# Kernel tuning notes

Measured on AMD Instinct MI355X. Metric: run time of the kernel, lower is better.

The kernel has to match this reference:

```python
import jax, jax.numpy as jnp
import numpy as np

N_NODES = 100000
N_EDGES = 1600000
NUM_FEATURES = 128
HIDDEN = 64
NUM_CLASSES = 16


def setup_inputs() -> dict:
    key = jax.random.key(0)
    k1, k2, k3, k4 = jax.random.split(key, 4)
    x = jax.random.normal(k1, (N_NODES, NUM_FEATURES), dtype=jnp.float32)
    edge_index = jax.random.randint(k2, (2, N_EDGES), 0, N_NODES, dtype=jnp.int64)
    # Glorot-ish scaled weights ([in, out] layout; PyG stores [out,in] but math is x @ W)
    W1 = jax.random.normal(k3, (NUM_FEATURES, HIDDEN), dtype=jnp.float32) * (1.0 / np.sqrt(NUM_FEATURES))
    W2 = jax.random.normal(k4, (HIDDEN, NUM_CLASSES), dtype=jnp.float32) * (1.0 / np.sqrt(HIDDEN))
    return {"x": x, "edge_index": edge_index, "W1": W1, "W2": W2}


def _gcn_conv(x, edge_index, W):
    # GCNConv(add_self_loops=False, bias=False): linear then sym-normalized scatter-add.
    n = x.shape[0]
    row, col = edge_index[0], edge_index[1]  # source -> target
    h = x @ W  # [N, out]
    # degree from unit edge weights scattered on target nodes
    deg = jax.ops.segment_sum(jnp.ones(row.shape[0], dtype=h.dtype), col, num_segments=n)
    deg_inv_sqrt = jnp.where(deg > 0, jax.lax.rsqrt(jnp.maximum(deg, 1.0)), 0.0)
    norm = deg_inv_sqrt[row] * deg_inv_sqrt[col]  # [E]
    msg = h[row] * norm[:, None]  # gather + scale, [E, out]
    return jax.ops.segment_sum(msg, col, num_segments=n)  # scatter-add to targets


def reference(x, edge_index, W1, W2):
    h = _gcn_conv(x, edge_index, W1)
    h = _gcn_conv(h, edge_index, W2)
    return jax.nn.log_softmax(h, axis=1)
```

## Files before the change

### kernel.cpp

```cpp
#include <hip/hip_runtime.h>
#include <hip/hip_bf16.h>
#include <hip/hip_fp16.h>


#define STRIDE 48
#define BCAP   3072


__global__ __launch_bounds__(256) void k_bucket(const int* __restrict__ ei,
                                                const void* __restrict__ xv,
                                                const void* __restrict__ W1v,
                                                const void* __restrict__ W2v,
                                                int* __restrict__ flags,
                                                float* __restrict__ W12,
                                                int* __restrict__ bcnt,
                                                int* __restrict__ buf,
                                                int e, int n, int nb) {
    __shared__ int hist[1024];
    __shared__ int basec[1024];
    __shared__ float wtmp[2048];
    __shared__ int sraw, sbad;
    int t = threadIdx.x;
    int b = blockIdx.x;

    if (t == 0) { sraw = 0; sbad = 0; }
    for (int i = t; i < nb; i += 256) hist[i] = 0;
    __syncthreads();

    {
        int i = b * 2048 + t;
        if (i < e && ei[2 * (size_t)i + 1] != 0) atomicOr(&sraw, 1);
    }
    if (b < 8) {
        const unsigned short* xs = (const unsigned short*)xv;
        int bad = 0;
        for (int i = t; i < 1024; i += 256) {
            unsigned ex2 = (xs[i] >> 7) & 0xFF;
            if (ex2 >= 0x90) bad = 1;
        }
        if (bad) atomicOr(&sbad, 1);
    }
    __syncthreads();
    int raw = sraw ? 0 : 1;

    if (b < 8) {
        bool f32 = sbad != 0;
        if (f32) {
            const float* W1 = (const float*)W1v;
            const float* W2 = (const float*)W2v;
            for (int i = t; i < 1024; i += 256) {
                wtmp[i] = W1[b * 1024 + i];
                wtmp[1024 + i] = W2[i];
            }
        } else {
            const __hip_bfloat16* W1 = (const __hip_bfloat16*)W1v;
            const __hip_bfloat16* W2 = (const __hip_bfloat16*)W2v;
            for (int i = t; i < 1024; i += 256) {
                wtmp[i] = __bfloat162float(W1[b * 1024 + i]);
                wtmp[1024 + i] = __bfloat162float(W2[i]);
            }
        }
    }

    int e0 = b * 2048;
    int bk[8], rec[8];
#pragma unroll
    for (int j = 0; j < 8; ++j) {
        int i = e0 + j * 256 + t;
        bk[j] = -1;
        if (i < e) {
            int r, c;
            if (raw) {
                r = ((const int2*)ei)[(size_t)i].x;
                c = ((const int2*)ei)[(size_t)e + i].x;
            } else {
                r = ei[i];
                c = ei[(size_t)e + i];
            }
            if ((unsigned)c < (unsigned)n && (unsigned)r < (unsigned)n) {
                bk[j] = c >> 7;
                rec[j] = ((c & 127) << 17) | r;
                atomicAdd(&hist[bk[j]], 1);
            }
        }
    }
    __syncthreads();

    if (b < 8) {
        int kl = t >> 4, c = t & 15;
        float acc = 0.0f;
#pragma unroll 8
        for (int f = 0; f < 64; ++f) acc += wtmp[kl * 64 + f] * wtmp[1024 + f * 16 + c];
        W12[(16 * b + kl) * 16 + c] = acc;
        if (b == 0 && t == 0) { flags[0] = sbad; flags[1] = raw; }
    }

    for (int i = t; i < nb; i += 256) {
        int h = hist[i];
        basec[i] = h ? atomicAdd(&bcnt[i], h) : 0;
    }
    __syncthreads();
#pragma unroll
    for (int j = 0; j < 8; ++j) {
        if (bk[j] >= 0) {
            int slot = atomicAdd(&basec[bk[j]], 1);
            if (slot < BCAP) buf[(size_t)bk[j] * BCAP + slot] = rec[j];
        }
    }
}


__global__ __launch_bounds__(256) void k_csr_z(const int* __restrict__ bcnt,
                                               const int* __restrict__ buf,
                                               const void* __restrict__ xv,
                                               const float* __restrict__ W12,
                                               const int* __restrict__ flags,
                                               int* __restrict__ cnt,
                                               int* __restrict__ csr,
                                               __half* __restrict__ z, int n) {
    __shared__ int lcnt[128];
    __shared__ int lcsr[128 * STRIDE];
    __shared__ float ws[2048];
    int t = threadIdx.x;
    int b = blockIdx.x;
    if (t < 128) lcnt[t] = 0;
    int4 zero4 = {0, 0, 0, 0};
    for (int i = t; i < 128 * STRIDE / 4; i += 256) ((int4*)lcsr)[i] = zero4;
    for (int i = t; i < 2048; i += 256) ws[i] = W12[i];
    __syncthreads();

    int m = bcnt[b];
    if (m > BCAP) m = BCAP;
    for (int i = t; i < m; i += 256) {
        int rec = buf[(size_t)b * BCAP + i];
        int cl = rec >> 17;
        int r = rec & 0x1FFFF;
        int slot = atomicAdd(&lcnt[cl], 1);
        if (slot < STRIDE) lcsr[cl * STRIDE + slot] = r;
    }
    __syncthreads();

    {
        int node = (b << 7) + t;
        if (t < 128 && node < n) cnt[node] = lcnt[t];
    }
    const int4* src = (const int4*)lcsr;
    int4* dst = (int4*)csr + (size_t)b * (128 * STRIDE / 4);
    for (int i = t; i < 128 * STRIDE / 4; i += 256) dst[i] = src[i];

    int node_l = t >> 1;
    int kh = t & 1;
    int node0 = (b << 7) + node_l;
    if (node0 >= n) return;
    int node = node0;

    float acc[16];
#pragma unroll
    for (int c = 0; c < 16; ++c) acc[c] = 0.0f;

    if (flags[0]) {
        const float4* x4 = (const float4*)xv + (size_t)node * 32 + kh * 16;
#pragma unroll
        for (int j = 0; j < 16; ++j) {
            float4 v = x4[j];
            float xk[4] = {v.x, v.y, v.z, v.w};
#pragma unroll
            for (int q = 0; q < 4; ++q) {
                const float* w = &ws[(kh * 64 + j * 4 + q) * 16];
                float xx = xk[q];
#pragma unroll
                for (int c = 0; c < 16; ++c) acc[c] += xx * w[c];
            }
        }
    } else {
        const uint4* x4 = (const uint4*)xv + (size_t)node * 16 + kh * 8;
#pragma unroll
        for (int j = 0; j < 8; ++j) {
            uint4 v = x4[j];
            float xk[8];
            xk[0] = __uint_as_float(v.x << 16);
            xk[1] = __uint_as_float(v.x & 0xffff0000u);
            xk[2] = __uint_as_float(v.y << 16);
            xk[3] = __uint_as_float(v.y & 0xffff0000u);
            xk[4] = __uint_as_float(v.z << 16);
            xk[5] = __uint_as_float(v.z & 0xffff0000u);
            xk[6] = __uint_as_float(v.w << 16);
            xk[7] = __uint_as_float(v.w & 0xffff0000u);
#pragma unroll
            for (int q = 0; q < 8; ++q) {
                const float* w = &ws[(kh * 64 + j * 8 + q) * 16];
                float xx = xk[q];
#pragma unroll
                for (int c = 0; c < 16; ++c) acc[c] += xx * w[c];
            }
        }
    }

#pragma unroll
    for (int c = 0; c < 16; ++c) acc[c] += __shfl_xor(acc[c], 1);

    int deg = lcnt[node_l];
    float di = (deg > 0) ? rsqrtf((float)deg) : 0.0f;
    int c0 = kh * 8;
    __half2 hh[4];
#pragma unroll
    for (int j = 0; j < 4; ++j)
        hh[j] = __halves2half2(__float2half(acc[c0 + 2 * j] * di),
                               __float2half(acc[c0 + 2 * j + 1] * di));
    uint4 u;
    u.x = *(unsigned*)&hh[0]; u.y = *(unsigned*)&hh[1];
    u.z = *(unsigned*)&hh[2]; u.w = *(unsigned*)&hh[3];
    ((uint4*)(z + (size_t)node * 16))[kh] = u;
}


__global__ __launch_bounds__(256) void k_agg1b(const int* __restrict__ cnt,
                                               const int* __restrict__ csr,
                                               const __half* __restrict__ z,
                                               __half* __restrict__ z2, int n) {
    int t = threadIdx.x;
    int wid = t >> 6, lane = t & 63;
    int half = lane >> 5, l5 = lane & 31;
    int node0 = blockIdx.x * 8 + wid * 2 + half;
    int node = node0 < n ? node0 : n - 1;
    int id  = csr[(size_t)node * STRIDE + l5];
    int id2 = csr[(size_t)node * STRIDE + 32 + (l5 & 15)];
    int deg = cnt[node];
    float di = (deg > 0) ? rsqrtf((float)deg) : 0.0f;
    int m = deg < STRIDE ? deg : STRIDE;
    int sub = l5 >> 3, f2 = l5 & 7;
    int base = half << 5;
    const __half2* zp = (const __half2*)z;
    float ax = 0.0f, ay = 0.0f;
#pragma unroll
    for (int j = 0; j < 24; j += 4) {
        int s = __shfl(id, base + j + sub);
        float2 v = __half22float2(zp[(size_t)s * 8 + f2]);
        bool ok = (j + sub) < m;
        ax += ok ? v.x : 0.0f;
        ay += ok ? v.y : 0.0f;
    }
    for (int j = 24; j < m; j += 4) {
        int sidx = j + sub;
        int s = (j < 32) ? __shfl(id, base + sidx)
                         : __shfl(id2, base + (sidx & 15));
        if (sidx < m) {
            float2 v = __half22float2(zp[(size_t)s * 8 + f2]);
            ax += v.x;
            ay += v.y;
        }
    }
    ax += __shfl_xor(ax, 8);  ay += __shfl_xor(ay, 8);
    ax += __shfl_xor(ax, 16); ay += __shfl_xor(ay, 16);
    float s2 = di * di;
    if (node0 < n && l5 < 8)
        ((__half2*)z2)[(size_t)node * 8 + l5] =
            __halves2half2(__float2half(ax * s2), __float2half(ay * s2));
}


__global__ __launch_bounds__(256) void k_agg2b(const int* __restrict__ cnt,
                                               const int* __restrict__ csr,
                                               const __half* __restrict__ z2,
                                               const int* __restrict__ flags,
                                               void* __restrict__ outv, int n) {
    int t = threadIdx.x;
    int wid = t >> 6, lane = t & 63;
    int half = lane >> 5, l5 = lane & 31;
    int node0 = blockIdx.x * 8 + wid * 2 + half;
    int node = node0 < n ? node0 : n - 1;
    int id  = csr[(size_t)node * STRIDE + l5];
    int id2 = csr[(size_t)node * STRIDE + 32 + (l5 & 15)];
    int deg = cnt[node];
    float di = (deg > 0) ? rsqrtf((float)deg) : 0.0f;
    int m = deg < STRIDE ? deg : STRIDE;
    int sub = l5 >> 3, f2 = l5 & 7;
    int base = half << 5;
    const __half2* zp = (const __half2*)z2;
    float ax = 0.0f, ay = 0.0f;
#pragma unroll
    for (int j = 0; j < 24; j += 4) {
        int s = __shfl(id, base + j + sub);
        float2 v = __half22float2(zp[(size_t)s * 8 + f2]);
        bool ok = (j + sub) < m;
        ax += ok ? v.x : 0.0f;
        ay += ok ? v.y : 0.0f;
    }
    for (int j = 24; j < m; j += 4) {
        int sidx = j + sub;
        int s = (j < 32) ? __shfl(id, base + sidx)
                         : __shfl(id2, base + (sidx & 15));
        if (sidx < m) {
            float2 v = __half22float2(zp[(size_t)s * 8 + f2]);
            ax += v.x;
            ay += v.y;
        }
    }
    ax += __shfl_xor(ax, 8);  ay += __shfl_xor(ay, 8);
    ax += __shfl_xor(ax, 16); ay += __shfl_xor(ay, 16);
    float vx = ax * di, vy = ay * di;
    float mx = fmaxf(vx, vy);
#pragma unroll
    for (int d = 1; d <= 4; d <<= 1) mx = fmaxf(mx, __shfl_xor(mx, d));
    float es = __expf(vx - mx) + __expf(vy - mx);
#pragma unroll
    for (int d = 1; d <= 4; d <<= 1) es += __shfl_xor(es, d);
    float ls = __logf(es);
    float rx = vx - mx - ls, ry = vy - mx - ls;
    if (node0 < n && l5 < 8) {
        if (flags[0]) {
            float2 r; r.x = rx; r.y = ry;
            ((float2*)outv)[(size_t)node * 8 + l5] = r;
        } else {
            __hip_bfloat162 hh;
            hh.x = __float2bfloat16(rx);
            hh.y = __float2bfloat16(ry);
            ((__hip_bfloat162*)outv)[(size_t)node * 8 + l5] = hh;
        }
    }
}


extern "C" void kernel_launch(void* const* d_in, const int* in_sizes, int n_in,
                              void* d_out, int out_size, void* d_ws, size_t ws_size,
                              hipStream_t stream) {
    const int F = 128, C = 16;
    int n = in_sizes[0] / F;
    int e = in_sizes[1] / 2;
    int nb = (n + 127) >> 7;

    const void* x = d_in[0];
    const int* ei = (const int*)d_in[1];
    const void* W1 = d_in[2];
    const void* W2 = d_in[3];

    char* p = (char*)d_ws;
    auto carve = [&](size_t bytes) {
        char* r = p;
        p += (bytes + 255) & ~(size_t)255;
        return r;
    };
    int*    flags = (int*)  carve(256);
    int*    bcnt  = (int*)  carve((size_t)nb * 4);
    int*    cnt   = (int*)  carve((size_t)n * 4);
    float*  W12   = (float*)carve(128 * 16 * 4);
    int*    csr   = (int*)  carve(((size_t)nb * 128 * STRIDE + 64) * 4);
    __half* z     = (__half*)carve((size_t)n * C * 2);
    size_t buf_sz = (size_t)nb * BCAP * 4;
    size_t z2_sz = (size_t)n * C * 2;
    char* regionB = carve(buf_sz > z2_sz ? buf_sz : z2_sz);
    int*    buf = (int*)regionB;
    __half* z2  = (__half*)regionB;
    (void)ws_size;

    int gb_bucket = (e + 2047) / 2048;
    if (gb_bucket < 8) gb_bucket = 8;

    hipMemsetAsync(bcnt, 0, (size_t)nb * 4, stream);
    k_bucket<<<gb_bucket, 256, 0, stream>>>(ei, x, W1, W2, flags, W12, bcnt, buf, e, n, nb);
    k_csr_z<<<nb, 256, 0, stream>>>(bcnt, buf, x, W12, flags, cnt, csr, z, n);
    k_agg1b<<<(n + 7) / 8, 256, 0, stream>>>(cnt, csr, z, z2, n);
    k_agg2b<<<(n + 7) / 8, 256, 0, stream>>>(cnt, csr, z2, flags, d_out, n);
}
```

Before: 181.0 us.

## Sort edges by bucket in shared memory before writing to global buckets

The bucketing kernel now uses 1024-thread blocks, each handling about 6272 edges. It counting-sorts the edge records by destination bucket in LDS, using a block-wide prefix scan, and then writes them to global memory in bucket-contiguous runs. This is meant to replace scattered per-edge global stores with more coalesced writes and to cut the number of global atomics on bucket counters. In exchange it adds a 10-step scan with barriers, more shared memory per block and fewer blocks, which may reduce occupancy.

```diff
diff --git a/kernel.cpp b/kernel.cpp
--- a/kernel.cpp
+++ b/kernel.cpp
@@ -5,40 +5,47 @@
 
 #define STRIDE 48
 #define BCAP   3072
-
-
-__global__ __launch_bounds__(256) void k_bucket(const int* __restrict__ ei,
-                                                const void* __restrict__ xv,
-                                                const void* __restrict__ W1v,
-                                                const void* __restrict__ W2v,
-                                                int* __restrict__ flags,
-                                                float* __restrict__ W12,
-                                                int* __restrict__ bcnt,
-                                                int* __restrict__ buf,
-                                                int e, int n, int nb) {
+#define SRTCAP 6272
+
+
+__global__ __launch_bounds__(1024) void k_bucket(const int* __restrict__ ei,
+                                                 const void* __restrict__ xv,
+                                                 const void* __restrict__ W1v,
+                                                 const void* __restrict__ W2v,
+                                                 int* __restrict__ flags,
+                                                 float* __restrict__ W12,
+                                                 int* __restrict__ bcnt,
+                                                 int* __restrict__ buf,
+                                                 int e, int n, int nb, int epb) {
     __shared__ int hist[1024];
-    __shared__ int basec[1024];
+    __shared__ int scn[1024];
+    __shared__ int cur[1024];
+    __shared__ int gb[1024];
     __shared__ float wtmp[2048];
-    __shared__ int sraw, sbad;
+    __shared__ int srt[SRTCAP];
+    __shared__ unsigned short key[SRTCAP];
+    __shared__ int sraw, sbad, tot;
     int t = threadIdx.x;
     int b = blockIdx.x;
 
     if (t == 0) { sraw = 0; sbad = 0; }
-    for (int i = t; i < nb; i += 256) hist[i] = 0;
-    __syncthreads();
-
-    {
-        int i = b * 2048 + t;
-        if (i < e && ei[2 * (size_t)i + 1] != 0) atomicOr(&sraw, 1);
+    hist[t] = 0;
+    __syncthreads();
+
+    long long base_e = (long long)b * epb;
+    int myE = e - (int)base_e;
+    if (myE > epb) myE = epb;
+
+    if (t < myE) {
+        long long i = base_e + t;
+        if (ei[2 * (size_t)i + 1] != 0) atomicOr(&sraw, 1);
     }
     if (b < 8) {
         const unsigned short* xs = (const unsigned short*)xv;
-        int bad = 0;
-        for (int i = t; i < 1024; i += 256) {
-            unsigned ex2 = (xs[i] >> 7) & 0xFF;
-            if (ex2 >= 0x90) bad = 1;
-        }
-        if (bad) atomicOr(&sbad, 1);
+        if (t < 1024) {
+            unsigned ex2 = (xs[t] >> 7) & 0xFF;
+            if (ex2 >= 0x90) atomicOr(&sbad, 1);
+        }
     }
     __syncthreads();
     int raw = sraw ? 0 : 1;
@@ -48,27 +55,23 @@
         if (f32) {
             const float* W1 = (const float*)W1v;
             const float* W2 = (const float*)W2v;
-            for (int i = t; i < 1024; i += 256) {
-                wtmp[i] = W1[b * 1024 + i];
-                wtmp[1024 + i] = W2[i];
-            }
+            wtmp[t] = W1[b * 1024 + t];
+            wtmp[1024 + t] = W2[t];
         } else {
             const __hip_bfloat16* W1 = (const __hip_bfloat16*)W1v;
             const __hip_bfloat16* W2 = (const __hip_bfloat16*)W2v;
-            for (int i = t; i < 1024; i += 256) {
-                wtmp[i] = __bfloat162float(W1[b * 1024 + i]);
-                wtmp[1024 + i] = __bfloat162float(W2[i]);
-            }
-        }
-    }
-
-    int e0 = b * 2048;
-    int bk[8], rec[8];
-#pragma unroll
-    for (int j = 0; j < 8; ++j) {
-        int i = e0 + j * 256 + t;
+            wtmp[t] = __bfloat162float(W1[b * 1024 + t]);
+            wtmp[1024 + t] = __bfloat162float(W2[t]);
+        }
+    }
+
+    int bk[7], rec[7];
+#pragma unroll
+    for (int j = 0; j < 7; ++j) {
+        int li = j * 1024 + t;
         bk[j] = -1;
-        if (i < e) {
+        if (li < myE) {
+            long long i = base_e + li;
             int r, c;
             if (raw) {
                 r = ((const int2*)ei)[(size_t)i].x;
@@ -86,26 +89,48 @@
     }
     __syncthreads();
 
-    if (b < 8) {
+    scn[t] = hist[t];
+    __syncthreads();
+#pragma unroll
+    for (int off = 1; off < 1024; off <<= 1) {
+        int add = (t >= off) ? scn[t - off] : 0;
+        __syncthreads();
+        scn[t] += add;
+        __syncthreads();
+    }
+    {
+        int h = hist[t];
+        cur[t] = scn[t] - h;
+        gb[t] = h ? atomicAdd(&bcnt[t], h) : 0;
+        if (t == 1023) tot = scn[1023];
+    }
+    __syncthreads();
+
+#pragma unroll
+    for (int j = 0; j < 7; ++j) {
+        if (bk[j] >= 0) {
+            int s = atomicAdd(&cur[bk[j]], 1);
+            srt[s] = rec[j];
+            key[s] = (unsigned short)bk[j];
+        }
+    }
+    __syncthreads();
+
+    int total = tot;
+    for (int i = t; i < total; i += 1024) {
+        int k = key[i];
+        int excl = cur[k] - hist[k];
+        int slot = gb[k] + (i - excl);
+        if (slot < BCAP) buf[(size_t)k * BCAP + slot] = srt[i];
+    }
+
+    if (b < 8 && t < 256) {
         int kl = t >> 4, c = t & 15;
         float acc = 0.0f;
 #pragma unroll 8
         for (int f = 0; f < 64; ++f) acc += wtmp[kl * 64 + f] * wtmp[1024 + f * 16 + c];
         W12[(16 * b + kl) * 16 + c] = acc;
         if (b == 0 && t == 0) { flags[0] = sbad; flags[1] = raw; }
-    }
-
-    for (int i = t; i < nb; i += 256) {
-        int h = hist[i];
-        basec[i] = h ? atomicAdd(&bcnt[i], h) : 0;
-    }
-    __syncthreads();
-#pragma unroll
-    for (int j = 0; j < 8; ++j) {
-        if (bk[j] >= 0) {
-            int slot = atomicAdd(&basec[bk[j]], 1);
-            if (slot < BCAP) buf[(size_t)bk[j] * BCAP + slot] = rec[j];
-        }
     }
 }
 
@@ -353,11 +378,12 @@
     __half* z2  = (__half*)regionB;
     (void)ws_size;
 
-    int gb_bucket = (e + 2047) / 2048;
-    if (gb_bucket < 8) gb_bucket = 8;
+    int gb_bucket = (e + SRTCAP - 1) / SRTCAP;
+    if (gb_bucket < 256) gb_bucket = 256;
+    int epb = (e + gb_bucket - 1) / gb_bucket;
 
     hipMemsetAsync(bcnt, 0, (size_t)nb * 4, stream);
-    k_bucket<<<gb_bucket, 256, 0, stream>>>(ei, x, W1, W2, flags, W12, bcnt, buf, e, n, nb);
+    k_bucket<<<gb_bucket, 1024, 0, stream>>>(ei, x, W1, W2, flags, W12, bcnt, buf, e, n, nb, epb);
     k_csr_z<<<nb, 256, 0, stream>>>(bcnt, buf, x, W12, flags, cnt, csr, z, n);
     k_agg1b<<<(n + 7) / 8, 256, 0, stream>>>(cnt, csr, z, z2, n);
     k_agg2b<<<(n + 7) / 8, 256, 0, stream>>>(cnt, csr, z2, flags, d_out, n);
```

Result: faster. 159.8 us, median of 2 (-11.7%).
